# Kernel optimization log

Hardware: AMD Instinct MI355X
Metric: run time of the kernel (lower is better)

The kernel has to match this reference:

```python
import jax, jax.numpy as jnp
import numpy as np

N, P, M, J, H = 32768, 5, 1024, 24, 256
SMPL_THRESH = 0.08


def _rand_transforms(rng, n):
    # random small-angle rotations + small translations -> invertible 4x4 joint transforms
    axis = rng.normal(size=(n, 3))
    axis /= np.linalg.norm(axis, axis=-1, keepdims=True)
    ang = rng.uniform(-0.5, 0.5, size=(n, 1, 1))
    K = np.zeros((n, 3, 3))
    K[:, 0, 1] = -axis[:, 2]; K[:, 0, 2] = axis[:, 1]
    K[:, 1, 0] = axis[:, 2];  K[:, 1, 2] = -axis[:, 0]
    K[:, 2, 0] = -axis[:, 1]; K[:, 2, 1] = axis[:, 0]
    R = np.eye(3)[None] + np.sin(ang) * K + (1.0 - np.cos(ang)) * (K @ K)
    T = np.zeros((n, 4, 4))
    T[:, :3, :3] = R
    T[:, :3, 3] = rng.normal(size=(n, 3)) * 0.1
    T[:, 3, 3] = 1.0
    return T.astype(np.float32)


def setup_inputs() -> dict:
    key = jax.random.key(0)
    ks = jax.random.split(key, 12)
    rng = np.random.default_rng(0)
    pose_pts = jax.random.normal(ks[0], (1, N, 3), jnp.float32) * 0.5
    pose_dirs = jax.random.normal(ks[1], (1, N, 3), jnp.float32)
    pose_dirs = pose_dirs / jnp.linalg.norm(pose_dirs, axis=-1, keepdims=True)
    part_pts = jax.random.normal(ks[2], (P, M, 3), jnp.float32) * 0.5
    part_pbw = jax.nn.softmax(jax.random.normal(ks[3], (P, M, J), jnp.float32), axis=-1)
    A = jnp.asarray(_rand_transforms(rng, J))[None]       # [1,24,4,4]
    big_A = jnp.asarray(_rand_transforms(rng, J))[None]   # [1,24,4,4]
    W1 = jax.random.normal(ks[4], (3, H), jnp.float32) * 0.1
    b1 = jnp.zeros((H,), jnp.float32)
    W2 = jax.random.normal(ks[5], (H, H), jnp.float32) * 0.06
    b2 = jnp.zeros((H,), jnp.float32)
    W3 = jax.random.normal(ks[6], (H, 3), jnp.float32) * 0.06
    b3 = jnp.zeros((3,), jnp.float32)
    lengths2 = jnp.full((P,), M, dtype=jnp.int32)
    return {"pose_pts": pose_pts, "pose_dirs": pose_dirs, "part_pts": part_pts,
            "part_pbw": part_pbw, "A": A, "big_A": big_A,
            "W1": W1, "b1": b1, "W2": W2, "b2": b2, "W3": W3, "b3": b3,
            "lengths2": lengths2}


def _lbs_pipeline(pose_pts, pose_dirs, part_pts, part_pbw, A, big_A,
                  W1, b1, W2, b2, W3, b3, lengths2):
    # ---- KNN (K=1) blend-weight lookup per part (torch.no_grad block) ----
    x = pose_pts[0]                                              # [N,3]
    d2 = (jnp.sum(x * x, -1)[:, None, None]
          - 2.0 * jnp.einsum('nd,pmd->npm', x, part_pts)
          + jnp.sum(part_pts * part_pts, -1)[None])              # [N,P,M]
    valid = jnp.arange(M)[None, :] < lengths2[:, None]           # [P,M]
    d2 = jnp.where(valid[None], jnp.maximum(d2, 0.0), jnp.inf)
    nn = jnp.argmin(d2, axis=-1)                                 # [N,P]
    pnorm = jnp.sqrt(jnp.take_along_axis(d2, nn[..., None], -1)[..., 0])  # [N,P]
    bw = part_pbw[jnp.arange(P)[None, :], nn]                    # [N,P,24]
    bw = jax.lax.stop_gradient(bw)
    pnorm = jax.lax.stop_gradient(pnorm)
    pflag = pnorm < SMPL_THRESH                                  # [N,P]

    # ---- gather-expand: each point assigned to every part ----
    pts_e = jnp.broadcast_to(x[:, None, :], (N, P, 3)).reshape(N * P, 3)
    dirs_e = jnp.broadcast_to(pose_dirs[0][:, None, :], (N, P, 3)).reshape(N * P, 3)
    bw_f = bw.reshape(N * P, J)

    # ---- per-point inverse linear blend skinning ----
    A_bw = jnp.einsum('kj,jxy->kxy', bw_f, A[0])                 # [NP,4,4]
    R_inv = jnp.linalg.inv(A_bw[:, :3, :3])
    tpts = jnp.einsum('kxy,ky->kx', R_inv, pts_e - A_bw[:, :3, 3])
    Ab = jnp.einsum('kj,jxy->kxy', bw_f, big_A[0])               # [NP,4,4]
    Rb = Ab[:, :3, :3]
    init_bigpose = jnp.einsum('kxy,ky->kx', Rb, tpts) + Ab[:, :3, 3]
    tdirs = jnp.einsum('kxy,ky->kx', R_inv, dirs_e)
    tpose_dirs = jnp.einsum('kxy,ky->kx', Rb, tdirs).reshape(1, N, P, 3)

    # ---- tpose deformer (residual MLP, masked by part flag) ----
    h = jax.nn.relu(init_bigpose @ W1 + b1)
    h = jax.nn.relu(h @ W2 + b2)
    resd = 0.05 * jnp.tanh(h @ W3 + b3)
    resd = resd * pflag.reshape(N * P, 1).astype(resd.dtype)
    tpose = (init_bigpose + resd).reshape(1, N, P, 3)
    return (tpose, tpose_dirs, resd.reshape(1, N, P, 3),
            pflag.reshape(1, N, P), init_bigpose[None], pnorm[None])


def reference(pose_pts, pose_dirs, part_pts, part_pbw, A, big_A,
              W1, b1, W2, b2, W3, b3, lengths2):
    return _lbs_pipeline(pose_pts, pose_dirs, part_pts, part_pbw, A, big_A,
                         W1, b1, W2, b2, W3, b3, lengths2)
```

## Files before the change

### kernel.cpp

```cpp
#include <hip/hip_runtime.h>
#include <stdint.h>
#include <math.h>

#define NPTS 32768
#define PP   5
#define MM   1024
#define JJ   24
#define HH   256

#define O0 0
#define O1 491520
#define O2 983040
#define O3 1474560
#define O4 1638400
#define O5 2129920

typedef unsigned short ushort_t;
typedef unsigned int   uint_t;
typedef unsigned long long u64_t;
typedef __attribute__((ext_vector_type(8))) short bf16x8;
typedef __attribute__((ext_vector_type(4))) float f32x4;
typedef __attribute__((ext_vector_type(2))) float f32x2;

__device__ __forceinline__ ushort_t f2bf(float f) {
  union { uint_t i; float f; } v; v.f = f;
  uint_t i = v.i;
  return (ushort_t)((i + 0x7FFFu + ((i >> 16) & 1u)) >> 16);
}
__device__ __forceinline__ uint_t cvt_pk_bf16(float lo, float hi) {
  uint_t r;
  asm("v_cvt_pk_bf16_f32 %0, %1, %2" : "=v"(r) : "v"(lo), "v"(hi));
  return r;
}
__device__ __forceinline__ float tanh_fast(float v) {
  v = fminf(fmaxf(v, -15.f), 15.f);
  float e = __expf(2.f*v);
  return __fdividef(e - 1.f, e + 1.f);
}

__device__ __forceinline__ void transform_one(
    int n, int p, int nn, float pn, float fl,
    float px, float py, float pz, float dx, float dy, float dz,
    const float* __restrict__ pbw,
    const float4* __restrict__ sA4, const float4* __restrict__ sB4,
    float* __restrict__ out)
{
  const float4* bwr = (const float4*)(pbw + ((size_t)p * MM + nn) * JJ);
  float bw[24];
  #pragma unroll
  for (int q = 0; q < 6; ++q) {
    float4 u = bwr[q];
    bw[q*4+0] = u.x; bw[q*4+1] = u.y; bw[q*4+2] = u.z; bw[q*4+3] = u.w;
  }

  float M1[12], M2[12];
  #pragma unroll
  for (int q = 0; q < 12; ++q) { M1[q] = 0.f; M2[q] = 0.f; }
  #pragma unroll
  for (int j = 0; j < 24; ++j) {
    float w = bw[j];
    float4 a0 = sA4[j*3+0], a1 = sA4[j*3+1], a2 = sA4[j*3+2];
    M1[0]=fmaf(w,a0.x,M1[0]); M1[1]=fmaf(w,a0.y,M1[1]); M1[2]=fmaf(w,a0.z,M1[2]); M1[3]=fmaf(w,a0.w,M1[3]);
    M1[4]=fmaf(w,a1.x,M1[4]); M1[5]=fmaf(w,a1.y,M1[5]); M1[6]=fmaf(w,a1.z,M1[6]); M1[7]=fmaf(w,a1.w,M1[7]);
    M1[8]=fmaf(w,a2.x,M1[8]); M1[9]=fmaf(w,a2.y,M1[9]); M1[10]=fmaf(w,a2.z,M1[10]); M1[11]=fmaf(w,a2.w,M1[11]);
    float4 c0 = sB4[j*3+0], c1 = sB4[j*3+1], c2 = sB4[j*3+2];
    M2[0]=fmaf(w,c0.x,M2[0]); M2[1]=fmaf(w,c0.y,M2[1]); M2[2]=fmaf(w,c0.z,M2[2]); M2[3]=fmaf(w,c0.w,M2[3]);
    M2[4]=fmaf(w,c1.x,M2[4]); M2[5]=fmaf(w,c1.y,M2[5]); M2[6]=fmaf(w,c1.z,M2[6]); M2[7]=fmaf(w,c1.w,M2[7]);
    M2[8]=fmaf(w,c2.x,M2[8]); M2[9]=fmaf(w,c2.y,M2[9]); M2[10]=fmaf(w,c2.z,M2[10]); M2[11]=fmaf(w,c2.w,M2[11]);
  }
  float a=M1[0], b=M1[1], c=M1[2];
  float d=M1[4], e=M1[5], f=M1[6];
  float g=M1[8], h=M1[9], i=M1[10];
  float C00 = e*i - f*h, C01 = c*h - b*i, C02 = b*f - c*e;
  float C10 = f*g - d*i, C11 = a*i - c*g, C12 = c*d - a*f;
  float C20 = d*h - e*g, C21 = b*g - a*h, C22 = a*e - b*d;
  float det = a*C00 + b*C10 + c*C20;
  float rd = 1.0f / det;
  float tx = px - M1[3], ty = py - M1[7], tz = pz - M1[11];
  float t0 = rd * (C00*tx + C01*ty + C02*tz);
  float t1 = rd * (C10*tx + C11*ty + C12*tz);
  float t2 = rd * (C20*tx + C21*ty + C22*tz);
  float i0 = M2[0]*t0 + M2[1]*t1 + M2[2]*t2  + M2[3];
  float i1 = M2[4]*t0 + M2[5]*t1 + M2[6]*t2  + M2[7];
  float i2 = M2[8]*t0 + M2[9]*t1 + M2[10]*t2 + M2[11];
  float d0 = rd * (C00*dx + C01*dy + C02*dz);
  float d1 = rd * (C10*dx + C11*dy + C12*dz);
  float d2 = rd * (C20*dx + C21*dy + C22*dz);
  float e0 = M2[0]*d0 + M2[1]*d1 + M2[2]*d2;
  float e1 = M2[4]*d0 + M2[5]*d1 + M2[6]*d2;
  float e2 = M2[8]*d0 + M2[9]*d1 + M2[10]*d2;

  size_t k = (size_t)n * PP + p;
  out[O1 + k*3+0] = e0; out[O1 + k*3+1] = e1; out[O1 + k*3+2] = e2;
  out[O3 + k] = fl;
  out[O4 + k*3+0] = i0; out[O4 + k*3+1] = i1; out[O4 + k*3+2] = i2;
  out[O5 + k] = pn;
}

__global__ __launch_bounds__(256) void nn_kernel(
    const float* __restrict__ pp0, const float* __restrict__ pp1,
    const float* __restrict__ part_pts, const float* __restrict__ pbw,
    const float* __restrict__ Ag, const float* __restrict__ Bg,
    const int* __restrict__ lengths2,
    const float* __restrict__ W2g, ushort_t* __restrict__ W2bf,
    float* __restrict__ out)
{
  if (blockIdx.x >= 1280) {
    int k = blockIdx.x - 1280;
    int n = threadIdx.x;
    float v = W2g[k*256 + n];
    int kc = k >> 5, quad = (k & 31) >> 3, j = k & 7;
    int tile = n >> 4, lane = quad*16 + (n & 15);
    W2bf[kc*8192 + tile*512 + lane*8 + j] = f2bf(v);
    return;
  }

  __shared__ float4 sXq[256], sYq[256], sZq[256], sWq[256];
  __shared__ float4 sA4[72];
  __shared__ float4 sB4[72];
  int t = threadIdx.x;
  int p  = blockIdx.x >> 8;
  int nb = blockIdx.x & 255;
  int g  = t >> 3;
  int s  = t & 7;
  int n0 = nb*128 + g*4;

  float s0r0 = pp0[0], s0r1 = pp0[1], s0r2 = pp0[2];
  float nrm = s0r0*s0r0 + s0r1*s0r1 + s0r2*s0r2;
  bool c0_is_dirs = fabsf(nrm - 1.0f) < 1e-4f;
  const float* pose_pts  = c0_is_dirs ? pp1 : pp0;
  const float* pose_dirs = c0_is_dirs ? pp0 : pp1;

  {
    #pragma clang fp contract(off)
    float* fX = (float*)sXq; float* fY = (float*)sYq;
    float* fZ = (float*)sZq; float* fW = (float*)sWq;
    for (int i = t; i < MM; i += 256) {
      float x = part_pts[((size_t)p*MM+i)*3+0];
      float y = part_pts[((size_t)p*MM+i)*3+1];
      float z = part_pts[((size_t)p*MM+i)*3+2];
      float yy = ((x*x) + (y*y)) + (z*z);
      fX[i] = x; fY[i] = y; fZ[i] = z; fW[i] = yy;
    }
  }
  for (int i = t; i < 72; i += 256) {
    int l = i*4;
    int j = l / 12, rc = l % 12;
    float4 qa, qb;
    qa.x = Ag[j*16+rc+0]; qa.y = Ag[j*16+rc+1]; qa.z = Ag[j*16+rc+2]; qa.w = Ag[j*16+rc+3];
    qb.x = Bg[j*16+rc+0]; qb.y = Bg[j*16+rc+1]; qb.z = Bg[j*16+rc+2]; qb.w = Bg[j*16+rc+3];
    sA4[i] = qa; sB4[i] = qb;
  }
  int mlen = lengths2[p]; if (mlen > MM) mlen = MM;
  __syncthreads();

  float X[4], Y[4], Z[4];
  f32x2 Xd[4], Yd[4], Zd[4], C2[4];
  {
    #pragma clang fp contract(off)
    const float4* pr = (const float4*)(pose_pts + (size_t)n0*3);
    float4 f0 = pr[0], f1 = pr[1], f2 = pr[2];
    X[0]=f0.x; Y[0]=f0.y; Z[0]=f0.z;
    X[1]=f0.w; Y[1]=f1.x; Z[1]=f1.y;
    X[2]=f1.z; Y[2]=f1.w; Z[2]=f2.x;
    X[3]=f2.y; Y[3]=f2.z; Z[3]=f2.w;
    #pragma unroll
    for (int j = 0; j < 4; ++j) {
      float x2 = ((X[j]*X[j]) + (Y[j]*Y[j])) + (Z[j]*Z[j]);
      Xd[j] = (f32x2){2.0f*X[j], 2.0f*X[j]};
      Yd[j] = (f32x2){2.0f*Y[j], 2.0f*Y[j]};
      Zd[j] = (f32x2){2.0f*Z[j], 2.0f*Z[j]};
      C2[j] = (f32x2){x2, x2};
    }
  }

  float best[4] = {INFINITY, INFINITY, INFINITY, INFINITY};
  int   code[4] = {0, 0, 0, 0};
  {
    #pragma clang fp contract(off)
    int nq = mlen >> 5;
    for (int k = 0; k < nq; ++k) {
      int qi = k*8 + s;
      float4 QX = sXq[qi], QY = sYq[qi], QZ = sZq[qi], QW = sWq[qi];
      f32x2 qx0 = {QX.x, QX.y}, qx1 = {QX.z, QX.w};
      f32x2 qy0 = {QY.x, QY.y}, qy1 = {QY.z, QY.w};
      f32x2 qz0 = {QZ.x, QZ.y}, qz1 = {QZ.z, QZ.w};
      f32x2 qw0 = {QW.x, QW.y}, qw1 = {QW.z, QW.w};
      int cb = k << 2;
      #pragma unroll
      for (int j = 0; j < 4; ++j) {
        f32x2 dt0 = ((Xd[j]*qx0) + (Yd[j]*qy0)) + (Zd[j]*qz0);
        f32x2 tt0 = (C2[j] - dt0) + qw0;
        f32x2 dt1 = ((Xd[j]*qx1) + (Yd[j]*qy1)) + (Zd[j]*qz1);
        f32x2 tt1 = (C2[j] - dt1) + qw1;
        float e0 = fmaxf(tt0.x, 0.f);
        float e1 = fmaxf(tt0.y, 0.f);
        float e2 = fmaxf(tt1.x, 0.f);
        float e3 = fmaxf(tt1.y, 0.f);
        bool l0 = e0 < best[j]; best[j] = fminf(best[j], e0); code[j] = l0 ? cb       : code[j];
        bool l1 = e1 < best[j]; best[j] = fminf(best[j], e1); code[j] = l1 ? (cb | 1) : code[j];
        bool l2 = e2 < best[j]; best[j] = fminf(best[j], e2); code[j] = l2 ? (cb | 2) : code[j];
        bool l3 = e3 < best[j]; best[j] = fminf(best[j], e3); code[j] = l3 ? (cb | 3) : code[j];
      }
    }
    int mb0 = nq << 5;
    if (mb0 < mlen) {
      const float* fX = (const float*)sXq; const float* fY = (const float*)sYq;
      const float* fZ = (const float*)sZq; const float* fW = (const float*)sWq;
      #pragma unroll
      for (int e = 0; e < 4; ++e) {
        int m = mb0 + 4*s + e;
        if (m < mlen) {
          float qx = fX[m], qy = fY[m], qz = fZ[m], qw = fW[m];
          int cc = (nq << 2) | e;
          #pragma unroll
          for (int j = 0; j < 4; ++j) {
            float dt2 = ((Xd[j].x*qx) + (Yd[j].x*qy)) + (Zd[j].x*qz);
            float dd = fmaxf((C2[j].x - dt2) + qw, 0.0f);
            bool lt = dd < best[j];
            best[j] = fminf(best[j], dd);
            code[j] = lt ? cc : code[j];
          }
        }
      }
    }
  }

  u64_t pk[4];
  #pragma unroll
  for (int j = 0; j < 4; ++j) {
    int mj = ((code[j] >> 2) << 5) + 4*s + (code[j] & 3);
    pk[j] = ((u64_t)__float_as_uint(best[j]) << 32) | (uint_t)mj;
    u64_t o;
    o = __shfl_xor(pk[j], 1); if (o < pk[j]) pk[j] = o;
    o = __shfl_xor(pk[j], 2); if (o < pk[j]) pk[j] = o;
    o = __shfl_xor(pk[j], 4); if (o < pk[j]) pk[j] = o;
  }

  if (s < 4) {
    u64_t mypk = (s==0) ? pk[0] : (s==1) ? pk[1] : (s==2) ? pk[2] : pk[3];
    float xa = (s==0) ? X[0] : (s==1) ? X[1] : (s==2) ? X[2] : X[3];
    float ya = (s==0) ? Y[0] : (s==1) ? Y[1] : (s==2) ? Y[2] : Y[3];
    float za = (s==0) ? Z[0] : (s==1) ? Z[1] : (s==2) ? Z[2] : Z[3];
    int n = n0 + s;
    int bm = (int)(mypk & 0xFFFFFFFFull);
    float bd = __uint_as_float((uint_t)(mypk >> 32));
    float pn = sqrtf(bd);
    float fl = ((double)pn < 0.08) ? 1.0f : 0.0f;
    float dxa = pose_dirs[n*3+0], dya = pose_dirs[n*3+1], dza = pose_dirs[n*3+2];
    transform_one(n, p, bm, pn, fl, xa, ya, za, dxa, dya, dza, pbw, sA4, sB4, out);
  }
}

__global__ __launch_bounds__(256) void mlp_kernel(
    const float* __restrict__ W1g, const float* __restrict__ b1g,
    const float* __restrict__ b2g, const float* __restrict__ W3g,
    const float* __restrict__ b3g, const ushort_t* __restrict__ W2bf,
    float* __restrict__ out)
{
  __shared__ float4 w1c[256];
  __shared__ float4 w3b2[256];

  int t = threadIdx.x;
  int wave = t >> 6, lane = t & 63, quad = lane >> 4, m16 = lane & 15;
  size_t row0 = (size_t)blockIdx.x * 64 + (size_t)wave * 16;

  {
    int c = t;
    w1c[c]  = make_float4(W1g[c], W1g[256+c], W1g[512+c], b1g[c]);
    w3b2[c] = make_float4(W3g[c*3+0], W3g[c*3+1], W3g[c*3+2], b2g[c]);
  }

  int r0 = (int)row0 + m16;
  float x0 = out[O4 + (size_t)r0*3+0], y0 = out[O4 + (size_t)r0*3+1], z0 = out[O4 + (size_t)r0*3+2];
  __syncthreads();

  f32x4 acc0[16];
  #pragma unroll
  for (int nt = 0; nt < 16; ++nt) acc0[nt] = (f32x4){0.f,0.f,0.f,0.f};

  const ushort_t* Wlane = W2bf + lane*8;
  #pragma unroll 1
  for (int kc = 0; kc < 8; ++kc) {
    const ushort_t* Bk = Wlane + kc*8192;
    bf16x8 Bcur[4], Bnxt[4];
    #pragma unroll
    for (int q = 0; q < 4; ++q) Bcur[q] = *(const bf16x8*)(Bk + q*512);

    union { bf16x8 v; uint_t u[4]; } ua0;
    int c0 = kc*32 + quad*8;
    #pragma unroll
    for (int jj = 0; jj < 4; ++jj) {
      float4 wA = w1c[c0 + 2*jj];
      float4 wB = w1c[c0 + 2*jj + 1];
      float hA0 = fmaxf(fmaf(z0, wA.z, fmaf(y0, wA.y, fmaf(x0, wA.x, wA.w))), 0.f);
      float hB0 = fmaxf(fmaf(z0, wB.z, fmaf(y0, wB.y, fmaf(x0, wB.x, wB.w))), 0.f);
      ua0.u[jj] = cvt_pk_bf16(hA0, hB0);
    }

    #pragma unroll
    for (int gq = 0; gq < 4; ++gq) {
      if (gq < 3) {
        #pragma unroll
        for (int q = 0; q < 4; ++q)
          Bnxt[q] = *(const bf16x8*)(Bk + (gq+1)*2048 + q*512);
      }
      #pragma unroll
      for (int q = 0; q < 4; ++q)
        acc0[gq*4+q] = __builtin_amdgcn_mfma_f32_16x16x32_bf16(ua0.v, Bcur[q], acc0[gq*4+q], 0, 0, 0);
      #pragma unroll
      for (int q = 0; q < 4; ++q) Bcur[q] = Bnxt[q];
    }
  }

  float flv = out[O3 + row0 + (size_t)m16];
  float ivx = out[O4 + (row0 + (size_t)m16)*3 + 0];
  float ivy = out[O4 + (row0 + (size_t)m16)*3 + 1];
  float ivz = out[O4 + (row0 + (size_t)m16)*3 + 2];

  float pr[4][3];
  #pragma unroll
  for (int reg = 0; reg < 4; ++reg) { pr[reg][0]=0.f; pr[reg][1]=0.f; pr[reg][2]=0.f; }
  #pragma unroll
  for (int nt = 0; nt < 16; ++nt) {
    float4 cv = w3b2[nt*16 + m16];
    #pragma unroll
    for (int reg = 0; reg < 4; ++reg) {
      float h2 = fmaxf(acc0[nt][reg] + cv.w, 0.f);
      pr[reg][0] = fmaf(h2, cv.x, pr[reg][0]);
      pr[reg][1] = fmaf(h2, cv.y, pr[reg][1]);
      pr[reg][2] = fmaf(h2, cv.z, pr[reg][2]);
    }
  }
  float b30 = b3g[0], b31 = b3g[1], b32 = b3g[2];
  #pragma unroll
  for (int reg = 0; reg < 4; ++reg) {
    float p0 = pr[reg][0], p1 = pr[reg][1], p2 = pr[reg][2];
    #pragma unroll
    for (int mask = 1; mask < 16; mask <<= 1) {
      p0 += __shfl_xor(p0, mask);
      p1 += __shfl_xor(p1, mask);
      p2 += __shfl_xor(p2, mask);
    }
    int src = quad*4 + reg;
    float fl = __shfl(flv, src);
    float i0 = __shfl(ivx, src);
    float i1 = __shfl(ivy, src);
    float i2 = __shfl(ivz, src);
    if (m16 == 0) {
      int r = (int)row0 + src;
      float rr0 = 0.05f * tanh_fast(p0 + b30) * fl;
      float rr1 = 0.05f * tanh_fast(p1 + b31) * fl;
      float rr2 = 0.05f * tanh_fast(p2 + b32) * fl;
      out[O0 + (size_t)r*3+0] = i0 + rr0;
      out[O0 + (size_t)r*3+1] = i1 + rr1;
      out[O0 + (size_t)r*3+2] = i2 + rr2;
      out[O2 + (size_t)r*3+0] = rr0;
      out[O2 + (size_t)r*3+1] = rr1;
      out[O2 + (size_t)r*3+2] = rr2;
    }
  }
}

extern "C" void kernel_launch(void* const* d_in, const int* in_sizes, int n_in,
                              void* d_out, int out_size, void* d_ws, size_t ws_size,
                              hipStream_t stream) {
  (void)out_size; (void)ws_size;
  const int want[13] = {98304, 98304, 15360, 122880, 384, 384, 768, 256, 65536, 256, 768, 3, 5};
  int idx[13];
  bool used[64] = {false};
  for (int L = 0; L < 13; ++L) {
    idx[L] = -1;
    for (int s = 0; s < n_in && s < 64; ++s) {
      if (!used[s] && in_sizes[s] == want[L]) { idx[L] = s; used[s] = true; break; }
    }
    if (idx[L] < 0) idx[L] = L;
  }
  const float* pp0       = (const float*)d_in[idx[0]];
  const float* pp1       = (const float*)d_in[idx[1]];
  const float* part_pts  = (const float*)d_in[idx[2]];
  const float* part_pbw  = (const float*)d_in[idx[3]];
  const float* A         = (const float*)d_in[idx[4]];
  const float* bigA      = (const float*)d_in[idx[5]];
  const float* W1        = (const float*)d_in[idx[6]];
  const float* b1        = (const float*)d_in[idx[7]];
  const float* W2        = (const float*)d_in[idx[8]];
  const float* b2        = (const float*)d_in[idx[9]];
  const float* W3        = (const float*)d_in[idx[10]];
  const float* b3        = (const float*)d_in[idx[11]];
  const int*   lengths2  = (const int*)d_in[idx[12]];
  float* out = (float*)d_out;
  ushort_t* W2bf = (ushort_t*)d_ws;

  nn_kernel<<<1536, 256, 0, stream>>>(pp0, pp1, part_pts, part_pbw,
                                      A, bigA, lengths2, W2, W2bf, out);
  mlp_kernel<<<2560, 256, 0, stream>>>(W1, b1, b2, W3, b3, W2bf, out);
}
```

Measured before the change: 183.7 us.

## Split MLP hidden columns across waves so each wave reuses W2 fragments over 64 rows

The MLP kernel used to give each wave 16 rows and have it stream all of W2 (256x256). Now each wave owns a quarter of the output columns for all 64 rows in the block, so each B fragment loaded is reused across four row tiles. This cuts global/L2 traffic on W2 by about four times. Layer-1 activations are recomputed per wave for all 64 rows. Partial layer-3 sums from the four waves are then reduced through shared memory, which adds a barrier and a final cooperative write stage.

```diff
diff --git a/kernel.cpp b/kernel.cpp
--- a/kernel.cpp
+++ b/kernel.cpp
@@ -260,10 +260,11 @@
 {
   __shared__ float4 w1c[256];
   __shared__ float4 w3b2[256];
+  __shared__ float  pp[64][4][3];
 
   int t = threadIdx.x;
   int wave = t >> 6, lane = t & 63, quad = lane >> 4, m16 = lane & 15;
-  size_t row0 = (size_t)blockIdx.x * 64 + (size_t)wave * 16;
+  size_t row0 = (size_t)blockIdx.x * 64;
 
   {
     int c = t;
@@ -271,93 +272,94 @@
     w3b2[c] = make_float4(W3g[c*3+0], W3g[c*3+1], W3g[c*3+2], b2g[c]);
   }
 
-  int r0 = (int)row0 + m16;
-  float x0 = out[O4 + (size_t)r0*3+0], y0 = out[O4 + (size_t)r0*3+1], z0 = out[O4 + (size_t)r0*3+2];
+  float xr[4], yr[4], zr[4];
+  #pragma unroll
+  for (int mt = 0; mt < 4; ++mt) {
+    size_t r = row0 + mt*16 + m16;
+    xr[mt] = out[O4 + r*3+0]; yr[mt] = out[O4 + r*3+1]; zr[mt] = out[O4 + r*3+2];
+  }
+
+  const ushort_t* Wlane = W2bf + (size_t)wave*4*512 + lane*8;
+  bf16x8 Bcur[4], Bnxt[4];
+  #pragma unroll
+  for (int q = 0; q < 4; ++q) Bcur[q] = *(const bf16x8*)(Wlane + q*512);
+
   __syncthreads();
 
-  f32x4 acc0[16];
-  #pragma unroll
-  for (int nt = 0; nt < 16; ++nt) acc0[nt] = (f32x4){0.f,0.f,0.f,0.f};
-
-  const ushort_t* Wlane = W2bf + lane*8;
+  f32x4 acc[16];
+  #pragma unroll
+  for (int i = 0; i < 16; ++i) acc[i] = (f32x4){0.f,0.f,0.f,0.f};
+
   #pragma unroll 1
   for (int kc = 0; kc < 8; ++kc) {
-    const ushort_t* Bk = Wlane + kc*8192;
-    bf16x8 Bcur[4], Bnxt[4];
-    #pragma unroll
-    for (int q = 0; q < 4; ++q) Bcur[q] = *(const bf16x8*)(Bk + q*512);
-
-    union { bf16x8 v; uint_t u[4]; } ua0;
+    union { bf16x8 v; uint_t u[4]; } ua[4];
     int c0 = kc*32 + quad*8;
     #pragma unroll
     for (int jj = 0; jj < 4; ++jj) {
       float4 wA = w1c[c0 + 2*jj];
       float4 wB = w1c[c0 + 2*jj + 1];
-      float hA0 = fmaxf(fmaf(z0, wA.z, fmaf(y0, wA.y, fmaf(x0, wA.x, wA.w))), 0.f);
-      float hB0 = fmaxf(fmaf(z0, wB.z, fmaf(y0, wB.y, fmaf(x0, wB.x, wB.w))), 0.f);
-      ua0.u[jj] = cvt_pk_bf16(hA0, hB0);
-    }
-
+      #pragma unroll
+      for (int mt = 0; mt < 4; ++mt) {
+        float hA = fmaxf(fmaf(zr[mt], wA.z, fmaf(yr[mt], wA.y, fmaf(xr[mt], wA.x, wA.w))), 0.f);
+        float hB = fmaxf(fmaf(zr[mt], wB.z, fmaf(yr[mt], wB.y, fmaf(xr[mt], wB.x, wB.w))), 0.f);
+        ua[mt].u[jj] = cvt_pk_bf16(hA, hB);
+      }
+    }
+    if (kc < 7) {
+      #pragma unroll
+      for (int q = 0; q < 4; ++q)
+        Bnxt[q] = *(const bf16x8*)(Wlane + (kc+1)*8192 + q*512);
+    }
     #pragma unroll
-    for (int gq = 0; gq < 4; ++gq) {
-      if (gq < 3) {
-        #pragma unroll
-        for (int q = 0; q < 4; ++q)
-          Bnxt[q] = *(const bf16x8*)(Bk + (gq+1)*2048 + q*512);
-      }
+    for (int mt = 0; mt < 4; ++mt)
       #pragma unroll
       for (int q = 0; q < 4; ++q)
-        acc0[gq*4+q] = __builtin_amdgcn_mfma_f32_16x16x32_bf16(ua0.v, Bcur[q], acc0[gq*4+q], 0, 0, 0);
+        acc[mt*4+q] = __builtin_amdgcn_mfma_f32_16x16x32_bf16(ua[mt].v, Bcur[q], acc[mt*4+q], 0, 0, 0);
+    if (kc < 7) {
       #pragma unroll
       for (int q = 0; q < 4; ++q) Bcur[q] = Bnxt[q];
     }
   }
 
-  float flv = out[O3 + row0 + (size_t)m16];
-  float ivx = out[O4 + (row0 + (size_t)m16)*3 + 0];
-  float ivy = out[O4 + (row0 + (size_t)m16)*3 + 1];
-  float ivz = out[O4 + (row0 + (size_t)m16)*3 + 2];
-
-  float pr[4][3];
-  #pragma unroll
-  for (int reg = 0; reg < 4; ++reg) { pr[reg][0]=0.f; pr[reg][1]=0.f; pr[reg][2]=0.f; }
-  #pragma unroll
-  for (int nt = 0; nt < 16; ++nt) {
-    float4 cv = w3b2[nt*16 + m16];
+  #pragma unroll
+  for (int mt = 0; mt < 4; ++mt) {
     #pragma unroll
     for (int reg = 0; reg < 4; ++reg) {
-      float h2 = fmaxf(acc0[nt][reg] + cv.w, 0.f);
-      pr[reg][0] = fmaf(h2, cv.x, pr[reg][0]);
-      pr[reg][1] = fmaf(h2, cv.y, pr[reg][1]);
-      pr[reg][2] = fmaf(h2, cv.z, pr[reg][2]);
-    }
-  }
-  float b30 = b3g[0], b31 = b3g[1], b32 = b3g[2];
-  #pragma unroll
-  for (int reg = 0; reg < 4; ++reg) {
-    float p0 = pr[reg][0], p1 = pr[reg][1], p2 = pr[reg][2];
-    #pragma unroll
-    for (int mask = 1; mask < 16; mask <<= 1) {
-      p0 += __shfl_xor(p0, mask);
-      p1 += __shfl_xor(p1, mask);
-      p2 += __shfl_xor(p2, mask);
-    }
-    int src = quad*4 + reg;
-    float fl = __shfl(flv, src);
-    float i0 = __shfl(ivx, src);
-    float i1 = __shfl(ivy, src);
-    float i2 = __shfl(ivz, src);
-    if (m16 == 0) {
-      int r = (int)row0 + src;
-      float rr0 = 0.05f * tanh_fast(p0 + b30) * fl;
-      float rr1 = 0.05f * tanh_fast(p1 + b31) * fl;
-      float rr2 = 0.05f * tanh_fast(p2 + b32) * fl;
-      out[O0 + (size_t)r*3+0] = i0 + rr0;
-      out[O0 + (size_t)r*3+1] = i1 + rr1;
-      out[O0 + (size_t)r*3+2] = i2 + rr2;
-      out[O2 + (size_t)r*3+0] = rr0;
-      out[O2 + (size_t)r*3+1] = rr1;
-      out[O2 + (size_t)r*3+2] = rr2;
+      float p0 = 0.f, p1 = 0.f, p2 = 0.f;
+      #pragma unroll
+      for (int q = 0; q < 4; ++q) {
+        float4 cv = w3b2[(wave*4+q)*16 + m16];
+        float h2 = fmaxf(acc[mt*4+q][reg] + cv.w, 0.f);
+        p0 = fmaf(h2, cv.x, p0);
+        p1 = fmaf(h2, cv.y, p1);
+        p2 = fmaf(h2, cv.z, p2);
+      }
+      #pragma unroll
+      for (int mask = 1; mask < 16; mask <<= 1) {
+        p0 += __shfl_xor(p0, mask);
+        p1 += __shfl_xor(p1, mask);
+        p2 += __shfl_xor(p2, mask);
+      }
+      if (m16 == 0) {
+        int lr = mt*16 + quad*4 + reg;
+        pp[lr][wave][0] = p0;
+        pp[lr][wave][1] = p1;
+        pp[lr][wave][2] = p2;
+      }
+    }
+  }
+  __syncthreads();
+
+  {
+    int lr = t >> 2, c = t & 3;
+    if (c < 3) {
+      float v = ((pp[lr][0][c] + pp[lr][1][c]) + pp[lr][2][c]) + pp[lr][3][c];
+      size_t r = row0 + lr;
+      float fl = out[O3 + r];
+      float iv = out[O4 + r*3 + c];
+      float rr = 0.05f * tanh_fast(v + b3g[c]) * fl;
+      out[O0 + r*3 + c] = iv + rr;
+      out[O2 + r*3 + c] = rr;
     }
   }
 }
```

New measurement: 184.8 us. Within noise of the previous version (+0.6%).
